# Optimization experiments

Measured on AMD Instinct MI355X. Metric: run time of the kernel, lower is better.

The kernel has to match this reference:

```python
import jax, jax.numpy as jnp
import numpy as np

K = 5          # knn_step1 = DenseDilatedKnnGraph(5, 1, ...)
BN_EPS = 1e-5  # torch BatchNorm2d default


def setup_inputs() -> dict:
    key = jax.random.key(0)
    k0, k1, k2 = jax.random.split(key, 3)
    B, C, H, W = 8, 128, 256, 256
    x = jax.random.normal(k0, (B, C, H, W), dtype=jnp.float32)
    # conv_seq params: 3x3 conv (no bias), BN affine, 1x1 conv (no bias)
    w1 = jax.random.normal(k1, (C, C, 3, 3), dtype=jnp.float32) * (1.0 / np.sqrt(C * 9))
    gamma = jnp.ones((C,), dtype=jnp.float32)
    beta = jnp.zeros((C,), dtype=jnp.float32)
    w2 = jax.random.normal(k2, (C, C, 1, 1), dtype=jnp.float32) * (1.0 / np.sqrt(C))
    return {"x": x, "w1": w1, "gamma": gamma, "beta": beta, "w2": w2}


def _forward(x, w1, gamma, beta, w2):
    B, C, H, W = x.shape  # H == W required by the original module
    # x_mean[b, n] = mean_{c,w} x[b,c,n,w] + mean_{c,h} x[b,c,h,n]   (B, N)
    xm = x.mean(axis=(1, 3)) + x.mean(axis=(1, 2))
    # DenseDilatedKnnGraph: L2-normalize along channel dim (C=1 -> sign),
    # pairwise sq-distance, top-k nearest (indices built under no_grad in torch)
    v = xm * 0.5
    s = v / jnp.maximum(jnp.abs(v), 1e-12)              # F.normalize, dim=1, C=1
    dist = (s[:, :, None] - s[:, None, :]) ** 2          # (B, N, N), feature dim 1
    _, nn_idx = jax.lax.top_k(-dist, K)                  # (B, N, K) nearest neighbors
    nn_idx = jax.lax.stop_gradient(nn_idx)
    # batched_index_select: gather node features at neighbor indices
    gathered = jax.vmap(lambda f, i: f[i])(xm, nn_idx)   # (B, N, K)
    gate = jax.nn.sigmoid(gathered.sum(axis=-1))         # (B, N)
    # x3.transpose(1,2) * x + x  ->  broadcast gate over channels and width
    y = gate[:, None, :, None] * x + x                   # (B, C, H, W)
    dn = ("NCHW", "OIHW", "NCHW")
    h = jax.lax.conv_general_dilated(y, w1, (1, 1), "SAME", dimension_numbers=dn)
    # BatchNorm2d, training-mode batch statistics (biased variance)
    mu = h.mean(axis=(0, 2, 3), keepdims=True)
    var = h.var(axis=(0, 2, 3), keepdims=True)
    h = (h - mu) * jax.lax.rsqrt(var + BN_EPS)
    h = h * gamma[None, :, None, None] + beta[None, :, None, None]
    h = jax.nn.relu(h)
    out = jax.lax.conv_general_dilated(h, w2, (1, 1), "SAME", dimension_numbers=dn)
    return out


def reference(x, w1, gamma, beta, w2):
    return _forward(x, w1, gamma, beta, w2)
```

## Files before the change

kernel.cpp:

```cpp
#include <hip/hip_runtime.h>
#include <hip/hip_bf16.h>
#include <math.h>

constexpr int B = 8, C = 128, H = 256, W = 256, NN = 256, KNN = 5;
constexpr int HW = H * W;

constexpr int WS_ROWSUM = 0;
constexpr int WS_COLSUM = 2048;
constexpr int WS_GMUL   = 4096;
constexpr int WS_SCALE  = 6144;
constexpr int WS_BIAS   = 6272;
constexpr int WS_PART   = 8192;
constexpr int WS_WT     = 24576;
constexpr int WS_W2T    = 98304;
constexpr size_t WS_Y_BYTES_OFF = 512 * 1024;

constexpr int Y2P_CS = 258 * 8;
constexpr int Y2P_HS = 16 * Y2P_CS;
constexpr int Y2P_BS = 258 * Y2P_HS;
constexpr size_t Y2P_BYTES = (size_t)B * Y2P_BS * 2;


typedef __attribute__((ext_vector_type(8))) short bf16x8;
typedef __attribute__((ext_vector_type(4))) float f32x4;

union U4 { uint4 q; bf16x8 v; unsigned short u[8]; };

typedef const __attribute__((address_space(1))) unsigned char* gas1;
typedef __attribute__((address_space(3))) unsigned char* las3;
__device__ __forceinline__ void gl_lds16(const void* g, void* l) {
    __builtin_amdgcn_global_load_lds((gas1)g, (las3)l, 16, 0, 0);
}

__device__ inline unsigned short f2bf(float f) {
    __hip_bfloat16 h = __float2bfloat16(f);
    return *reinterpret_cast<unsigned short*>(&h);
}
__device__ inline float bf2f(unsigned short u) {
    __hip_bfloat16 h = *reinterpret_cast<__hip_bfloat16*>(&u);
    return __bfloat162float(h);
}

__global__ __launch_bounds__(256) void k_sums(const float* __restrict__ x,
                                              float* __restrict__ ws) {
    const int b = blockIdx.x >> 7;
    const int c = blockIdx.x & 127;
    const int t = threadIdx.x;
    const int wv = t >> 6;
    const float4* p4 = (const float4*)(x + (size_t)(b * C + c) * HW);
    __shared__ float srow[256];
    __shared__ float scol[4][256];
    float ca0 = 0.f, ca1 = 0.f, ca2 = 0.f, ca3 = 0.f;
    for (int it = 0; it < 64; ++it) {
        const float4 v = p4[it * 256 + t];
        ca0 += v.x; ca1 += v.y; ca2 += v.z; ca3 += v.w;
        float s = v.x + v.y + v.z + v.w;
#pragma unroll
        for (int m = 1; m < 64; m <<= 1) s += __shfl_xor(s, m);
        if ((t & 63) == 0) srow[it * 4 + wv] = s;
    }
    const int cb = (t & 63) * 4;
    scol[wv][cb + 0] = ca0;
    scol[wv][cb + 1] = ca1;
    scol[wv][cb + 2] = ca2;
    scol[wv][cb + 3] = ca3;
    __syncthreads();
    atomicAdd(&ws[WS_ROWSUM + b * 256 + t], srow[t]);
    atomicAdd(&ws[WS_COLSUM + b * 256 + t],
              scol[0][t] + scol[1][t] + scol[2][t] + scol[3][t]);
}

__global__ void k_gate(float* __restrict__ ws) {
    const int b = blockIdx.x;
    const int i = threadIdx.x;
    __shared__ float xm[256], sgn[256];
    const float v = ws[WS_ROWSUM + b * 256 + i] * (1.f / 32768.f)
                  + ws[WS_COLSUM + b * 256 + i] * (1.f / 32768.f);
    xm[i] = v;
    const float vv = v * 0.5f;
    sgn[i] = vv / fmaxf(fabsf(vv), 1e-12f);
    __syncthreads();
    const float si = sgn[i];
    float bd[KNN];
    int bi[KNN];
    for (int k = 0; k < KNN; ++k) { bd[k] = 1e30f; bi[k] = 0; }
    for (int j = 0; j < NN; ++j) {
        float d = si - sgn[j];
        d *= d;
        if (d < bd[KNN - 1]) {
            int p = KNN - 1;
            while (p > 0 && bd[p - 1] > d) {
                bd[p] = bd[p - 1];
                bi[p] = bi[p - 1];
                --p;
            }
            bd[p] = d;
            bi[p] = j;
        }
    }
    float gs = 0.f;
    for (int k = 0; k < KNN; ++k) gs += xm[bi[k]];
    const float gate = 1.f / (1.f + expf(-gs));
    ws[WS_GMUL + b * 256 + i] = 1.f + gate;
}

__global__ __launch_bounds__(256) void k_yzero(unsigned short* __restrict__ y) {
    const int id = blockIdx.x * 256 + threadIdx.x;
    const uint4 z = {0u, 0u, 0u, 0u};
    if (id < 66048) {
        const int per = Y2P_HS / 8;
        const int b = id / (2 * per);
        const int r = id % (2 * per);
        const int hp = (r >= per) ? 257 : 0;
        const int off = (r >= per) ? r - per : r;
        *reinterpret_cast<uint4*>(y + (size_t)b * Y2P_BS + (size_t)hp * Y2P_HS + off * 8) = z;
    } else {
        const int id2 = id - 66048;
        const int b = id2 >> 13;
        const int r = id2 & 8191;
        const int hp = (r >> 5) + 1;
        const int c8 = (r >> 1) & 15;
        const int wp = (r & 1) ? 257 : 0;
        *reinterpret_cast<uint4*>(y + (size_t)b * Y2P_BS + (size_t)hp * Y2P_HS
                                  + c8 * Y2P_CS + wp * 8) = z;
    }
}

__global__ __launch_bounds__(256) void k_ygenT(const float* __restrict__ x,
                                               const float* __restrict__ ws,
                                               unsigned short* __restrict__ y) {
    const int b = blockIdx.x >> 8;
    const int h = blockIdx.x & 255;
    const int w = threadIdx.x;
    const float g = ws[WS_GMUL + b * 256 + h];
    const float* xp = x + ((size_t)(b * C) * H + h) * W + w;
    unsigned short* yp = y + (size_t)b * Y2P_BS + (size_t)(h + 1) * Y2P_HS + (w + 1) * 8;
    for (int c8 = 0; c8 < 16; ++c8) {
        U4 pk;
#pragma unroll
        for (int j = 0; j < 8; ++j)
            pk.u[j] = f2bf(xp[(size_t)(c8 * 8 + j) * HW] * g);
        *reinterpret_cast<uint4*>(yp + c8 * Y2P_CS) = pk.q;
    }
}

__global__ void k_wprep(const float* __restrict__ w1, unsigned short* __restrict__ wt) {
    const int e = blockIdx.x * 256 + threadIdx.x;
    const int j = e & 7;
    const int kg = (e >> 3) & 3;
    const int och = (e >> 5) & 127;
    const int s = e >> 12;
    const int c = (s & 3) * 32 + kg * 8 + j;
    const int pos = s >> 2;
    const int ky = pos / 3, kx = pos - ky * 3;
    wt[e] = f2bf(w1[(((size_t)och * C + c) * 3 + ky) * 3 + kx]);
}

__global__ void k_wprep2(const float* __restrict__ w2, unsigned short* __restrict__ w2t) {
    const int e = blockIdx.x * 256 + threadIdx.x;
    const int kk = e & 31;
    const int och = (e >> 5) & 127;
    const int s = e >> 12;
    w2t[e] = f2bf(w2[och * C + s * 32 + kk]);
}

__global__ __launch_bounds__(256) void k_conv3g(const unsigned short* __restrict__ y2,
                                                const unsigned short* __restrict__ wt,
                                                float* __restrict__ ws,
                                                float* __restrict__ hout) {
    const int bx0 = blockIdx.x;
    const int bx = (bx0 & 7) * 512 + (bx0 >> 3);
    const int whalf = bx & 1;
    const int hrow = (bx >> 1) & 255;
    const int b = bx >> 9;
    const int w0 = whalf * 128;

    const int t = threadIdx.x;
    const int wv = t >> 6;
    const int l = t & 63;
    const int wm = wv >> 1, wn = wv & 1;
    const int lr = l & 15, lq = l >> 4;

    __shared__ __attribute__((aligned(16))) unsigned short sA[2][4096];
    __shared__ __attribute__((aligned(16))) unsigned short sB[2][4096];
    __shared__ float sPart[4][128][2];

    f32x4 acc[4][4];
#pragma unroll
    for (int i = 0; i < 4; ++i)
#pragma unroll
        for (int j = 0; j < 4; ++j) acc[i][j] = (f32x4){0.f, 0.f, 0.f, 0.f};

    const char* wtb = (const char*)wt;
    const char* y2b = (const char*)y2 + (size_t)b * Y2P_BS * 2;
    const int k16s = (l & 3) ^ ((l >> 3) & 3);
    const unsigned aLane = (unsigned)((wv * 16 + (l >> 2)) * 64 + k16s * 16);
    const int pxl = wv * 16 + (l >> 2);
    const unsigned bLane0 = (unsigned)((pxl * 8 + k16s * Y2P_CS) * 2);
    const unsigned bLane1 = (unsigned)(((pxl + 64) * 8 + k16s * Y2P_CS) * 2);

    auto stage = [&](int s, char* sAp, char* sBp) {
        const int pos = s >> 2, cc = s & 3;
        const int ky = pos / 3, kx = pos - 3 * ky;
        const char* aSrc = wtb + ((size_t)s << 13);
        const char* bSrc = y2b + (size_t)((hrow + ky) * Y2P_HS + cc * 4 * Y2P_CS
                                          + (w0 + kx) * 8) * 2;
        gl_lds16(aSrc + aLane,        sAp + wv * 1024);
        gl_lds16(aSrc + 4096 + aLane, sAp + 4096 + wv * 1024);
        gl_lds16(bSrc + bLane0,       sBp + wv * 1024);
        gl_lds16(bSrc + bLane1,       sBp + 4096 + wv * 1024);
    };
    auto compute = [&](const unsigned short* aT, const unsigned short* bT) {
        const int lqs = lq ^ ((lr >> 1) & 3);
        const unsigned short* aRd = aT + (wm * 64 + lr) * 32 + lqs * 8;
        const unsigned short* bRd = bT + (wn * 64 + lr) * 32 + lqs * 8;
        bf16x8 af[4], bfr[4];
#pragma unroll
        for (int mf = 0; mf < 4; ++mf)
            af[mf] = *reinterpret_cast<const bf16x8*>(aRd + mf * 512);
#pragma unroll
        for (int nf = 0; nf < 4; ++nf)
            bfr[nf] = *reinterpret_cast<const bf16x8*>(bRd + nf * 512);
#pragma unroll
        for (int mf = 0; mf < 4; ++mf)
#pragma unroll
            for (int nf = 0; nf < 4; ++nf)
                acc[mf][nf] = __builtin_amdgcn_mfma_f32_16x16x32_bf16(
                    af[mf], bfr[nf], acc[mf][nf], 0, 0, 0);
    };

    stage(0, (char*)sA[0], (char*)sB[0]);
    __syncthreads();
    for (int s = 0; s < 36; s += 2) {
        if (s + 1 < 36) stage(s + 1, (char*)sA[1], (char*)sB[1]);
        compute(sA[0], sB[0]);
        __syncthreads();
        if (s + 2 < 36) stage(s + 2, (char*)sA[0], (char*)sB[0]);
        compute(sA[1], sB[1]);
        __syncthreads();
    }

#pragma unroll
    for (int mf = 0; mf < 4; ++mf) {
#pragma unroll
        for (int reg = 0; reg < 4; ++reg) {
            const int och = wm * 64 + mf * 16 + lq * 4 + reg;
            unsigned short* hseg = reinterpret_cast<unsigned short*>(
                hout + (((size_t)(b * C + och) * H + hrow) * W) + w0);
#pragma unroll
            for (int nf = 0; nf < 4; ++nf)
                hseg[wn * 64 + nf * 16 + lr] = f2bf(acc[mf][nf][reg]);
        }
    }

#pragma unroll
    for (int mf = 0; mf < 4; ++mf) {
#pragma unroll
        for (int reg = 0; reg < 4; ++reg) {
            float s = 0.f, q = 0.f;
#pragma unroll
            for (int nf = 0; nf < 4; ++nf) {
                const float v = acc[mf][nf][reg];
                s += v;
                q = fmaf(v, v, q);
            }
#pragma unroll
            for (int m = 1; m < 16; m <<= 1) {
                s += __shfl_xor(s, m);
                q += __shfl_xor(q, m);
            }
            if (lr == 0) {
                const int och = wm * 64 + mf * 16 + lq * 4 + reg;
                sPart[wv][och][0] = s;
                sPart[wv][och][1] = q;
            }
        }
    }
    __syncthreads();
    {
        const int o = t & 127;
        const int which = t >> 7;
        const int wmn = o >> 6;
        const float v = sPart[wmn * 2][o][which] + sPart[wmn * 2 + 1][o][which];
        atomicAdd(&ws[WS_PART + o * 128 + (bx & 63) * 2 + which], v);
    }
}

__device__ inline bf16x8 b_fetch(const float* __restrict__ x, int b, int s,
                                 int hrow, int w0, int px, int kg,
                                 float g0, float g1, float g2) {
    const int pos = s >> 2;
    const int ky = pos / 3, kx = pos - ky * 3;
    const int cbase = (s & 3) * 32 + kg * 8;
    int crow = hrow + ky - 1;
    int col = w0 + px + kx - 1;
    const float g = (ky == 0) ? g0 : ((ky == 1) ? g1 : g2);
    const float sc = ((unsigned)col < (unsigned)W) ? g : 0.f;
    crow = min(max(crow, 0), H - 1);
    col = min(max(col, 0), W - 1);
    const float* p = x + (((size_t)(b * C + cbase) * H + crow) * W + col);
    union { bf16x8 v8; unsigned short u[8]; } r;
#pragma unroll
    for (int j = 0; j < 8; ++j) r.u[j] = f2bf(p[(size_t)j * HW] * sc);
    return r.v8;
}

__global__ __launch_bounds__(256) void k_conv3(const float* __restrict__ x,
                                               const unsigned short* __restrict__ wt,
                                               float* __restrict__ ws,
                                               float* __restrict__ hout) {
    const int bx = blockIdx.x;
    const int whalf = bx & 1;
    const int hrow = (bx >> 1) & 255;
    const int b = bx >> 9;
    const int w0 = whalf * 128;

    const int t = threadIdx.x;
    const int wv = t >> 6;
    const int l = t & 63;
    const int wm = wv >> 1, wn = wv & 1;
    const int lr = l & 15, lq = l >> 4;

    __shared__ unsigned short sA[128 * 40];
    __shared__ unsigned short sB[128 * 40];
    __shared__ float sPart[4][128][2];

    float g0, g1, g2;
    {
        const int r0 = hrow - 1, r2 = hrow + 1;
        g0 = (r0 >= 0) ? ws[WS_GMUL + b * 256 + r0] : 0.f;
        g1 = ws[WS_GMUL + b * 256 + hrow];
        g2 = (r2 < H) ? ws[WS_GMUL + b * 256 + r2] : 0.f;
    }

    f32x4 acc[4][4];
#pragma unroll
    for (int i = 0; i < 4; ++i)
#pragma unroll
        for (int j = 0; j < 4; ++j) acc[i][j] = (f32x4){0.f, 0.f, 0.f, 0.f};

    const int a_och = t & 127, a_h = t >> 7;
    const int b_px = t & 127, b_kg0 = t >> 7;
    const int b_kg1 = b_kg0 + 2;

    uint4 pa0, pa1;
    bf16x8 pb0, pb1;
    {
        const uint4* asrc = reinterpret_cast<const uint4*>(wt + (size_t)a_och * 32 + a_h * 16);
        pa0 = asrc[0];
        pa1 = asrc[1];
        pb0 = b_fetch(x, b, 0, hrow, w0, b_px, b_kg0, g0, g1, g2);
        pb1 = b_fetch(x, b, 0, hrow, w0, b_px, b_kg1, g0, g1, g2);
    }

    for (int s = 0; s < 36; ++s) {
        __syncthreads();
        *reinterpret_cast<uint4*>(&sA[a_och * 40 + a_h * 16]) = pa0;
        *reinterpret_cast<uint4*>(&sA[a_och * 40 + a_h * 16 + 8]) = pa1;
        *reinterpret_cast<bf16x8*>(&sB[b_px * 40 + b_kg0 * 8]) = pb0;
        *reinterpret_cast<bf16x8*>(&sB[b_px * 40 + b_kg1 * 8]) = pb1;
        __syncthreads();

        if (s + 1 < 36) {
            const uint4* asrc = reinterpret_cast<const uint4*>(
                wt + (size_t)(s + 1) * 4096 + (size_t)a_och * 32 + a_h * 16);
            pa0 = asrc[0];
            pa1 = asrc[1];
            pb0 = b_fetch(x, b, s + 1, hrow, w0, b_px, b_kg0, g0, g1, g2);
            pb1 = b_fetch(x, b, s + 1, hrow, w0, b_px, b_kg1, g0, g1, g2);
        }

        bf16x8 af[4], bfr[4];
#pragma unroll
        for (int mf = 0; mf < 4; ++mf) {
            const int och = wm * 64 + mf * 16 + lr;
            af[mf] = *reinterpret_cast<const bf16x8*>(&sA[och * 40 + lq * 8]);
        }
#pragma unroll
        for (int nf = 0; nf < 4; ++nf) {
            const int px = wn * 64 + nf * 16 + lr;
            bfr[nf] = *reinterpret_cast<const bf16x8*>(&sB[px * 40 + lq * 8]);
        }
#pragma unroll
        for (int mf = 0; mf < 4; ++mf)
#pragma unroll
            for (int nf = 0; nf < 4; ++nf)
                acc[mf][nf] = __builtin_amdgcn_mfma_f32_16x16x32_bf16(
                    af[mf], bfr[nf], acc[mf][nf], 0, 0, 0);
    }

#pragma unroll
    for (int mf = 0; mf < 4; ++mf) {
#pragma unroll
        for (int reg = 0; reg < 4; ++reg) {
            const int och = wm * 64 + mf * 16 + lq * 4 + reg;
            unsigned short* hseg = reinterpret_cast<unsigned short*>(
                hout + (((size_t)(b * C + och) * H + hrow) * W) + w0);
#pragma unroll
            for (int nf = 0; nf < 4; ++nf)
                hseg[wn * 64 + nf * 16 + lr] = f2bf(acc[mf][nf][reg]);
        }
    }

#pragma unroll
    for (int mf = 0; mf < 4; ++mf) {
#pragma unroll
        for (int reg = 0; reg < 4; ++reg) {
            float s = 0.f, q = 0.f;
#pragma unroll
            for (int nf = 0; nf < 4; ++nf) {
                const float v = acc[mf][nf][reg];
                s += v;
                q = fmaf(v, v, q);
            }
#pragma unroll
            for (int m = 1; m < 16; m <<= 1) {
                s += __shfl_xor(s, m);
                q += __shfl_xor(q, m);
            }
            if (lr == 0) {
                const int och = wm * 64 + mf * 16 + lq * 4 + reg;
                sPart[wv][och][0] = s;
                sPart[wv][och][1] = q;
            }
        }
    }
    __syncthreads();
    {
        const int o = t & 127;
        const int which = t >> 7;
        const int wmn = o >> 6;
        const float v = sPart[wmn * 2][o][which] + sPart[wmn * 2 + 1][o][which];
        atomicAdd(&ws[WS_PART + o * 128 + (bx & 63) * 2 + which], v);
    }
}

__global__ void k_scalebias(const float* __restrict__ gamma,
                            const float* __restrict__ beta, float* __restrict__ ws) {
    const int c = threadIdx.x;
    const float* p = ws + WS_PART + c * 128;
    float s = 0.f, q = 0.f;
    for (int i = 0; i < 64; ++i) {
        s += p[i * 2];
        q += p[i * 2 + 1];
    }
    const float cnt = (float)B * HW;
    const float mu = s / cnt;
    const float var = q / cnt - mu * mu;
    const float rs = rsqrtf(var + 1e-5f);
    const float sc = rs * gamma[c];
    ws[WS_SCALE + c] = sc;
    ws[WS_BIAS + c] = beta[c] - mu * sc;
}

__global__ __launch_bounds__(256) void k_conv1d(float* __restrict__ io,
                                                const unsigned short* __restrict__ w2t,
                                                const float* __restrict__ ws) {
    const int bx = blockIdx.x;
    const int pblk = bx & 511;
    const int b = bx >> 9;
    const size_t p0 = (size_t)pblk * 128;

    const int t = threadIdx.x;
    const int wv = t >> 6;
    const int l = t & 63;
    const int wm = wv >> 1, wn = wv & 1;
    const int lr = l & 15, lq = l >> 4;

    __shared__ float sSB[128][2];
    if (t < 128) {
        sSB[t][0] = ws[WS_SCALE + t];
        sSB[t][1] = ws[WS_BIAS + t];
    }
    __syncthreads();

    f32x4 acc[4][4];
#pragma unroll
    for (int i = 0; i < 4; ++i)
#pragma unroll
        for (int j = 0; j < 4; ++j) acc[i][j] = (f32x4){0.f, 0.f, 0.f, 0.f};

    const unsigned aoff = (unsigned)((wm * 64 + lr) * 32 + lq * 8);
    const float* hbase_f = io + (size_t)b * C * HW + p0;
    const int segoff = wn * 64 + lr;

    uint4 pa0[4], pb0[4], pa1[4], pb1[4];

    auto loadA = [&](int s, uint4* d) {
        const unsigned so = aoff + (unsigned)(s * 4096);
#pragma unroll
        for (int mf = 0; mf < 4; ++mf)
            d[mf] = *reinterpret_cast<const uint4*>(w2t + so + mf * 512);
    };
    auto loadB = [&](int s, uint4* d) {
        const int c0 = s * 32 + lq * 8;
#pragma unroll
        for (int nf = 0; nf < 4; ++nf) {
            U4 fr;
#pragma unroll
            for (int j = 0; j < 8; ++j) {
                const unsigned short* hp = reinterpret_cast<const unsigned short*>(
                    hbase_f + (size_t)(c0 + j) * HW);
                const float v = fmaxf(
                    fmaf(bf2f(hp[segoff + nf * 16]), sSB[c0 + j][0], sSB[c0 + j][1]),
                    0.f);
                fr.u[j] = f2bf(v);
            }
            d[nf] = fr.q;
        }
    };
    auto mfma16 = [&](uint4* pa, uint4* pb) {
#pragma unroll
        for (int mf = 0; mf < 4; ++mf) {
            U4 am; am.q = pa[mf];
#pragma unroll
            for (int nf = 0; nf < 4; ++nf) {
                U4 bm; bm.q = pb[nf];
                acc[mf][nf] = __builtin_amdgcn_mfma_f32_16x16x32_bf16(
                    am.v, bm.v, acc[mf][nf], 0, 0, 0);
            }
        }
    };

    loadA(0, pa0);
    loadB(0, pb0);
    loadA(1, pa1);
    loadB(1, pb1);
    mfma16(pa0, pb0);
    loadA(2, pa0);
    loadB(2, pb0);
    mfma16(pa1, pb1);
    loadA(3, pa1);
    loadB(3, pb1);
    mfma16(pa0, pb0);
    mfma16(pa1, pb1);

    __syncthreads();

#pragma unroll
    for (int mf = 0; mf < 4; ++mf) {
#pragma unroll
        for (int reg = 0; reg < 4; ++reg) {
            const int och = wm * 64 + mf * 16 + lq * 4 + reg;
            float* orow = io + (size_t)(b * C + och) * HW + p0;
#pragma unroll
            for (int nf = 0; nf < 4; ++nf)
                orow[wn * 64 + nf * 16 + lr] = acc[mf][nf][reg];
        }
    }
}

extern "C" void kernel_launch(void* const* d_in, const int* in_sizes, int n_in,
                              void* d_out, int out_size, void* d_ws, size_t ws_size,
                              hipStream_t stream) {
    const float* x = (const float*)d_in[0];
    const float* w1 = (const float*)d_in[1];
    const float* gamma = (const float*)d_in[2];
    const float* beta = (const float*)d_in[3];
    const float* w2 = (const float*)d_in[4];
    float* out = (float*)d_out;
    float* ws = (float*)d_ws;
    unsigned short* wt = (unsigned short*)(ws + WS_WT);
    unsigned short* w2t = (unsigned short*)(ws + WS_W2T);

    hipMemsetAsync(d_ws, 0, 98304, stream);
    k_wprep<<<576, 256, 0, stream>>>(w1, wt);
    k_wprep2<<<64, 256, 0, stream>>>(w2, w2t);
    k_sums<<<B * C, 256, 0, stream>>>(x, ws);
    k_gate<<<B, 256, 0, stream>>>(ws);

    if (ws_size >= WS_Y_BYTES_OFF + Y2P_BYTES) {
        unsigned short* y2 = (unsigned short*)((char*)d_ws + WS_Y_BYTES_OFF);
        k_yzero<<<514, 256, 0, stream>>>(y2);
        k_ygenT<<<B * H, 256, 0, stream>>>(x, ws, y2);
        k_conv3g<<<B * 256 * 2, 256, 0, stream>>>(y2, wt, ws, out);
    } else {
        k_conv3<<<B * 256 * 2, 256, 0, stream>>>(x, wt, ws, out);
    }

    k_scalebias<<<1, 128, 0, stream>>>(gamma, beta, ws);
    k_conv1d<<<B * 512, 256, 0, stream>>>(out, w2t, ws);
}
```

Baseline: 508.7 us.

## Load conv weights directly to registers and deepen B-tile LDS pipeline

Result: slower. 520.8 us (+2.4%).

```diff
diff --git a/kernel.cpp b/kernel.cpp
--- a/kernel.cpp
+++ b/kernel.cpp
@@ -181,8 +181,7 @@
     const int wm = wv >> 1, wn = wv & 1;
     const int lr = l & 15, lq = l >> 4;
 
-    __shared__ __attribute__((aligned(16))) unsigned short sA[2][4096];
-    __shared__ __attribute__((aligned(16))) unsigned short sB[2][4096];
+    __shared__ __attribute__((aligned(16))) unsigned short sB[4][4096];
     __shared__ float sPart[4][128][2];
 
     f32x4 acc[4][4];
@@ -191,54 +190,69 @@
 #pragma unroll
         for (int j = 0; j < 4; ++j) acc[i][j] = (f32x4){0.f, 0.f, 0.f, 0.f};
 
-    const char* wtb = (const char*)wt;
     const char* y2b = (const char*)y2 + (size_t)b * Y2P_BS * 2;
     const int k16s = (l & 3) ^ ((l >> 3) & 3);
-    const unsigned aLane = (unsigned)((wv * 16 + (l >> 2)) * 64 + k16s * 16);
     const int pxl = wv * 16 + (l >> 2);
     const unsigned bLane0 = (unsigned)((pxl * 8 + k16s * Y2P_CS) * 2);
     const unsigned bLane1 = (unsigned)(((pxl + 64) * 8 + k16s * Y2P_CS) * 2);
-
-    auto stage = [&](int s, char* sAp, char* sBp) {
+    const unsigned short* aPtr = wt + (size_t)(wm * 64 + lr) * 32 + lq * 8;
+
+    auto stageB = [&](int s, char* sBp) {
         const int pos = s >> 2, cc = s & 3;
         const int ky = pos / 3, kx = pos - 3 * ky;
-        const char* aSrc = wtb + ((size_t)s << 13);
         const char* bSrc = y2b + (size_t)((hrow + ky) * Y2P_HS + cc * 4 * Y2P_CS
                                           + (w0 + kx) * 8) * 2;
-        gl_lds16(aSrc + aLane,        sAp + wv * 1024);
-        gl_lds16(aSrc + 4096 + aLane, sAp + 4096 + wv * 1024);
-        gl_lds16(bSrc + bLane0,       sBp + wv * 1024);
-        gl_lds16(bSrc + bLane1,       sBp + 4096 + wv * 1024);
+        gl_lds16(bSrc + bLane0, sBp + wv * 1024);
+        gl_lds16(bSrc + bLane1, sBp + 4096 + wv * 1024);
     };
-    auto compute = [&](const unsigned short* aT, const unsigned short* bT) {
+    auto loadA = [&](int s, uint4* d) {
+        const unsigned short* p = aPtr + (size_t)s * 4096;
+#pragma unroll
+        for (int mf = 0; mf < 4; ++mf)
+            d[mf] = *reinterpret_cast<const uint4*>(p + mf * 512);
+    };
+    auto compute = [&](const unsigned short* bT, uint4* aR) {
         const int lqs = lq ^ ((lr >> 1) & 3);
-        const unsigned short* aRd = aT + (wm * 64 + lr) * 32 + lqs * 8;
         const unsigned short* bRd = bT + (wn * 64 + lr) * 32 + lqs * 8;
-        bf16x8 af[4], bfr[4];
-#pragma unroll
-        for (int mf = 0; mf < 4; ++mf)
-            af[mf] = *reinterpret_cast<const bf16x8*>(aRd + mf * 512);
+        bf16x8 bfr[4];
 #pragma unroll
         for (int nf = 0; nf < 4; ++nf)
             bfr[nf] = *reinterpret_cast<const bf16x8*>(bRd + nf * 512);
 #pragma unroll
-        for (int mf = 0; mf < 4; ++mf)
+        for (int mf = 0; mf < 4; ++mf) {
+            U4 am; am.q = aR[mf];
 #pragma unroll
             for (int nf = 0; nf < 4; ++nf)
                 acc[mf][nf] = __builtin_amdgcn_mfma_f32_16x16x32_bf16(
-                    af[mf], bfr[nf], acc[mf][nf], 0, 0, 0);
+                    am.v, bfr[nf], acc[mf][nf], 0, 0, 0);
+        }
     };
 
-    stage(0, (char*)sA[0], (char*)sB[0]);
-    __syncthreads();
-    for (int s = 0; s < 36; s += 2) {
-        if (s + 1 < 36) stage(s + 1, (char*)sA[1], (char*)sB[1]);
-        compute(sA[0], sB[0]);
-        __syncthreads();
-        if (s + 2 < 36) stage(s + 2, (char*)sA[0], (char*)sB[0]);
-        compute(sA[1], sB[1]);
-        __syncthreads();
-    }
+    uint4 a0[4], a1[4];
+    stageB(0, (char*)sB[0]);
+    stageB(1, (char*)sB[1]);
+    loadA(0, a0);
+
+#define TILE_BODY(T, BUF, ASET_LD, ASET_CP, WAITN)                       \
+    {                                                                    \
+        if ((T) + 2 < 36) stageB((T) + 2, (char*)sB[((T) + 2) & 3]);     \
+        if ((T) + 1 < 36) loadA((T) + 1, ASET_LD);                       \
+        asm volatile("s_waitcnt vmcnt(" #WAITN ")" ::: "memory");        \
+        __builtin_amdgcn_s_barrier();                                    \
+        compute(sB[(BUF)], ASET_CP);                                     \
+    }
+
+    for (int s = 0; s < 32; s += 4) {
+        TILE_BODY(s + 0, (s + 0) & 3, a1, a0, 6)
+        TILE_BODY(s + 1, (s + 1) & 3, a0, a1, 6)
+        TILE_BODY(s + 2, (s + 2) & 3, a1, a0, 6)
+        TILE_BODY(s + 3, (s + 3) & 3, a0, a1, 6)
+    }
+    TILE_BODY(32, 0, a1, a0, 6)
+    TILE_BODY(33, 1, a0, a1, 6)
+    TILE_BODY(34, 2, a1, a0, 4)
+    TILE_BODY(35, 3, a0, a1, 0)
+#undef TILE_BODY
 
 #pragma unroll
     for (int mf = 0; mf < 4; ++mf) {
```
